# Optimization experiments

Hardware: AMD Instinct MI355X
Metric: run time of the kernel (lower is better)

## Reference

```python
import jax, jax.numpy as jnp
import numpy as np

EPS = 1e-12  # torch F.normalize eps

def _l2norm(t):
    # normalize along last axis, clamp norm like torch.nn.functional.normalize
    n = jnp.sqrt(jnp.sum(t * t, axis=-1, keepdims=True))
    return t / jnp.maximum(n, EPS)

def setup_inputs() -> dict:
    key = jax.random.key(0)
    k1, k2, k3 = jax.random.split(key, 3)
    B, N, C, h = 4, 16384, 512, 8
    x = jax.random.normal(k1, (B, N, C), dtype=jnp.float32)
    qkv_w = jax.random.normal(k2, (C, 3 * C), dtype=jnp.float32) * 0.02
    proj_w = jax.random.normal(k3, (C, C), dtype=jnp.float32) * 0.02
    proj_b = jnp.zeros((C,), dtype=jnp.float32)
    temperature = jnp.ones((h, 1, 1), dtype=jnp.float32)  # temperature_init=1.0
    return {"x": x, "H": 128, "W": 128, "qkv_w": qkv_w,
            "proj_w": proj_w, "proj_b": proj_b, "temperature": temperature}

def reference(x, H, W, qkv_w, proj_w, proj_b, temperature):
    B, N, C = x.shape
    h = temperature.shape[0]
    d = C // h
    qkv = (x @ qkv_w).reshape(B, N, 3, h, d)          # [B,N,3,h,d]
    qkv = jnp.transpose(qkv, (2, 0, 3, 1, 4))         # [3,B,h,N,d]
    q, k, v = qkv[0], qkv[1], qkv[2]
    # channel attention: transpose to [B,h,d,N], normalize over tokens
    q = _l2norm(jnp.swapaxes(q, -2, -1))              # [B,h,d,N]
    k = _l2norm(jnp.swapaxes(k, -2, -1))              # [B,h,d,N]
    v = jnp.swapaxes(v, -2, -1)                       # [B,h,d,N]
    attn = jnp.einsum('bhdn,bhen->bhde', q, k) * temperature  # [B,h,d,d]
    attn = jax.nn.softmax(attn, axis=-1)
    out = jnp.einsum('bhde,bhen->bhdn', attn, v)      # [B,h,d,N]
    out = jnp.transpose(out, (0, 3, 1, 2)).reshape(B, N, C)
    return out @ proj_w + proj_b
```

## Files before the change

### kernel.cpp

```cpp
#include <hip/hip_runtime.h>
#include <stdint.h>
#include <stddef.h>


typedef unsigned short u16;
typedef __attribute__((ext_vector_type(8))) unsigned short u16x8;
typedef __attribute__((ext_vector_type(8))) __bf16 bf16x8;
typedef __attribute__((ext_vector_type(4))) float f32x4;

#define B_DIM 4
#define N_TOK 16384
#define C_DIM 512
#define CQ3   1536
#define NROWS 65536

__device__ __forceinline__ u16 f2bf(float f) {
  union { float f; uint32_t u; } v; v.f = f;
  uint32_t r = v.u + 0x7FFFu + ((v.u >> 16) & 1u);
  return (u16)(r >> 16);
}
__device__ __forceinline__ float bf2f(u16 u) {
  union { uint32_t u; float f; } v; v.u = ((uint32_t)u) << 16;
  return v.f;
}
__device__ __forceinline__ bf16x8 as_bf16x8(u16x8 u) {
  union { u16x8 u; bf16x8 b; } v; v.u = u; return v.b;
}
__device__ __forceinline__ bf16x8 ldfrag(const u16* p) {
  return as_bf16x8(*(const u16x8*)p);
}
__device__ __forceinline__ void gl_lds16(const void* g, void* l) {
  __builtin_amdgcn_global_load_lds(
      (const __attribute__((address_space(1))) uint32_t*)g,
      (__attribute__((address_space(3))) uint32_t*)l, 16, 0, 0);
}
#define VMDRAIN asm volatile("s_waitcnt vmcnt(0)" ::: "memory")

__global__ __launch_bounds__(256) void k_prep(const float* __restrict__ qkv_w,
                                              const float* __restrict__ proj_w,
                                              u16* __restrict__ wl,
                                              u16* __restrict__ pwl,
                                              u16* __restrict__ vA) {
  int g = blockIdx.x * 256 + threadIdx.x;
  if (g < 98304) {
    int c8 = g / CQ3, j = g - c8 * CQ3;
    u16x8 o;
#pragma unroll
    for (int i = 0; i < 8; ++i) o[i] = f2bf(qkv_w[(size_t)(c8 * 8 + i) * CQ3 + j]);
    *(u16x8*)(wl + (size_t)g * 8) = o;
  } else if (g < 131072) {
    int gg = g - 98304;
    int d8 = gg >> 9, j = gg & 511;
    u16x8 o;
#pragma unroll
    for (int i = 0; i < 8; ++i) o[i] = f2bf(proj_w[(size_t)(d8 * 8 + i) * 512 + j]);
    *(u16x8*)(pwl + (size_t)gg * 8) = o;
  } else {
    int gg = g - 131072;
    int c = gg >> 6, q = gg & 63;
    const float* s = qkv_w + (size_t)c * CQ3 + 1024 + q * 8;
    float4 v0 = *(const float4*)s, v1 = *(const float4*)(s + 4);
    u16x8 o;
    o[0] = f2bf(v0.x); o[1] = f2bf(v0.y); o[2] = f2bf(v0.z); o[3] = f2bf(v0.w);
    o[4] = f2bf(v1.x); o[5] = f2bf(v1.y); o[6] = f2bf(v1.z); o[7] = f2bf(v1.w);
    *(u16x8*)(vA + (size_t)gg * 8) = o;
  }
}

__global__ __launch_bounds__(256) void k_xc(const float* __restrict__ x,
                                            u16* __restrict__ xb,
                                            u16* __restrict__ xbT) {
  __shared__ __align__(16) u16 T[16384];
  const int bi = blockIdx.x;
  const int b = bi >> 9, tt = (bi >> 2) & 127, ct = bi & 3;
  const int n0 = tt * 128, c0 = ct * 128;
  const int tid = threadIdx.x;
  const int cb8 = (tid & 15) * 8;
  const int tch = tid >> 4;
  const float* src = x + (size_t)(b * N_TOK + n0 + tch * 8) * C_DIM + c0 + cb8;
  float v[8][8];
#pragma unroll
  for (int j = 0; j < 8; ++j) {
    float4 a0 = *(const float4*)(src + (size_t)j * C_DIM);
    float4 a1 = *(const float4*)(src + (size_t)j * C_DIM + 4);
    v[j][0] = a0.x; v[j][1] = a0.y; v[j][2] = a0.z; v[j][3] = a0.w;
    v[j][4] = a1.x; v[j][5] = a1.y; v[j][6] = a1.z; v[j][7] = a1.w;
  }
  u16* xbd = xb + (size_t)(b * N_TOK + n0 + tch * 8) * C_DIM + c0 + cb8;
#pragma unroll
  for (int j = 0; j < 8; ++j) {
    u16x8 o;
#pragma unroll
    for (int i = 0; i < 8; ++i) o[i] = f2bf(v[j][i]);
    *(u16x8*)(xbd + (size_t)j * C_DIM) = o;
  }
#pragma unroll
  for (int i = 0; i < 8; ++i) {
    int c_loc = cb8 + i;
    int pc = tch ^ (tid & 15);
    u16x8 o;
#pragma unroll
    for (int j = 0; j < 8; ++j) o[j] = f2bf(v[j][i]);
    *(u16x8*)&T[c_loc * 128 + pc * 8] = o;
  }
  __syncthreads();
#pragma unroll
  for (int t = 0; t < 8; ++t) {
    int c_loc = t * 16 + (tid >> 4);
    int lch = tid & 15;
    int pc = lch ^ ((c_loc >> 3) & 15);
    u16x8 o = *(const u16x8*)&T[c_loc * 128 + pc * 8];
    *(u16x8*)&xbT[(size_t)(b * C_DIM + c0 + c_loc) * N_TOK + n0 + lch * 8] = o;
  }
}

__global__ __launch_bounds__(256) void k_g(const u16* __restrict__ xbT, u16* __restrict__ Gp) {
  __shared__ __align__(16) u16 As[2][8192];
  __shared__ __align__(16) u16 Bs[2][8192];
  const int tid = threadIdx.x, lane = tid & 63, wid = tid >> 6;
  const int orig = blockIdx.x;
  const int wg = (orig & 7) * 128 + (orig >> 3);
  const int kc = wg >> 6, rem = wg & 63;
  const int b = rem >> 4, ti = (rem >> 2) & 3, tj = rem & 3;
  const u16* abase = xbT + ((size_t)b * 512 + ti * 128) * N_TOK + kc * 1024;
  const u16* bbase = xbT + ((size_t)b * 512 + tj * 128) * N_TOK + kc * 1024;
  const int wr = wid >> 1, wc = wid & 1;

  const int sidx = tid >> 1, skblk0 = (tid & 1) * 4;

  auto stage = [&](int kb, int buf) {
#pragma unroll
    for (int s4 = 0; s4 < 4; ++s4) {
      int slot = s4 * 256 + tid;
      int idx = slot >> 3, kblk = slot & 7;
      int kcol = kb * 64 + ((kblk ^ (idx & 7)) * 8);
      gl_lds16(abase + (size_t)idx * N_TOK + kcol, &As[buf][slot * 8]);
      gl_lds16(bbase + (size_t)idx * N_TOK + kcol, &Bs[buf][slot * 8]);
    }
  };

  f32x4 acc[4][4];
#pragma unroll
  for (int i = 0; i < 4; ++i)
#pragma unroll
    for (int j = 0; j < 4; ++j) acc[i][j] = (f32x4){0.f, 0.f, 0.f, 0.f};

  stage(0, 0);
  VMDRAIN;
  __syncthreads();
  for (int kb = 0; kb < 16; ++kb) {
    const int cur = kb & 1;
    if (kb < 15) stage(kb + 1, cur ^ 1);
#pragma unroll
    for (int kk = 0; kk < 2; ++kk) {
      const int krow = kk * 4 + (lane >> 4);
      const int pk = krow ^ (lane & 7);
      bf16x8 af[4], bfr[4];
#pragma unroll
      for (int t = 0; t < 4; ++t)
        af[t] = *(const bf16x8*)&As[cur][((wr * 64 + t * 16 + (lane & 15)) * 8 + pk) * 8];
#pragma unroll
      for (int t = 0; t < 4; ++t)
        bfr[t] = *(const bf16x8*)&Bs[cur][((wc * 64 + t * 16 + (lane & 15)) * 8 + pk) * 8];
#pragma unroll
      for (int mt = 0; mt < 4; ++mt)
#pragma unroll
        for (int nt = 0; nt < 4; ++nt)
          acc[mt][nt] = __builtin_amdgcn_mfma_f32_16x16x32_bf16(af[mt], bfr[nt], acc[mt][nt], 0, 0, 0);
    }
    if (kb < 15) VMDRAIN;
    __syncthreads();
  }
  u16* wsl = &As[0][0] + wid * 4096;
#pragma unroll
  for (int mt = 0; mt < 4; ++mt)
#pragma unroll
    for (int nt = 0; nt < 4; ++nt)
#pragma unroll
      for (int r = 0; r < 4; ++r) {
        int row = mt * 16 + (lane >> 4) * 4 + r;
        int col = nt * 16 + (lane & 15);
        int slot = (col >> 3) ^ (row & 7);
        wsl[row * 64 + slot * 8 + (col & 7)] = f2bf(acc[mt][nt][r]);
      }
  u16* gdst = Gp + (size_t)(kc * 4 + b) * 262144;
#pragma unroll
  for (int it = 0; it < 8; ++it) {
    int rr = it * 8 + (lane >> 3);
    int slot = (lane & 7) ^ (rr & 7);
    *(u16x8*)&gdst[(size_t)(ti * 128 + wr * 64 + rr) * 512 + tj * 128 + wc * 64 + (lane & 7) * 8] =
        *(const u16x8*)&wsl[rr * 64 + slot * 8];
  }
}

__global__ __launch_bounds__(256) void k_red(const u16* __restrict__ Gp, u16* __restrict__ G) {
  int g = blockIdx.x * 256 + threadIdx.x;
  int b = g >> 15;
  size_t off = (size_t)(g & 32767) * 8;
  float s[8];
#pragma unroll
  for (int i = 0; i < 8; ++i) s[i] = 0.f;
  for (int kc = 0; kc < 16; ++kc) {
    u16x8 v = *(const u16x8*)(Gp + (size_t)(kc * 4 + b) * 262144 + off);
#pragma unroll
    for (int i = 0; i < 8; ++i) s[i] += bf2f(v[i]);
  }
  u16x8 o;
#pragma unroll
  for (int i = 0; i < 8; ++i) o[i] = f2bf(s[i]);
  *(u16x8*)(G + (size_t)b * 262144 + off) = o;
}

__global__ __launch_bounds__(256) void k_gq(const u16* __restrict__ G,
                                            const u16* __restrict__ wl,
                                            u16* __restrict__ Gqk) {
  const int bi = blockIdx.x;
  const int b = bi >> 5, mt = (bi >> 3) & 3, nt2 = bi & 7;
  const int m0 = mt * 128, n0 = nt2 * 128;
  const int lane = threadIdx.x & 63, w = threadIdx.x >> 6;
  f32x4 acc[8][2];
#pragma unroll
  for (int i = 0; i < 8; ++i) { acc[i][0] = (f32x4){0,0,0,0}; acc[i][1] = (f32x4){0,0,0,0}; }
  for (int ks = 0; ks < 16; ++ks) {
    bf16x8 bfr[2];
#pragma unroll
    for (int nf = 0; nf < 2; ++nf)
      bfr[nf] = ldfrag(wl + ((size_t)(ks * 4 + (lane >> 4)) * CQ3 + n0 + w * 32 + nf * 16 + (lane & 15)) * 8);
#pragma unroll
    for (int mf = 0; mf < 8; ++mf) {
      bf16x8 af = ldfrag(G + (size_t)b * 262144 + (size_t)(m0 + mf * 16 + (lane & 15)) * 512 + ks * 32 + (lane >> 4) * 8);
#pragma unroll
      for (int nf = 0; nf < 2; ++nf)
        acc[mf][nf] = __builtin_amdgcn_mfma_f32_16x16x32_bf16(af, bfr[nf], acc[mf][nf], 0, 0, 0);
    }
  }
#pragma unroll
  for (int mf = 0; mf < 8; ++mf)
#pragma unroll
    for (int nf = 0; nf < 2; ++nf)
#pragma unroll
      for (int r = 0; r < 4; ++r) {
        int d = m0 + mf * 16 + (lane >> 4) * 4 + r;
        int j = n0 + w * 32 + nf * 16 + (lane & 15);
        Gqk[(size_t)b * 524288 + ((size_t)(d >> 3) * 1024 + j) * 8 + (d & 7)] = f2bf(acc[mf][nf][r]);
      }
}

__global__ __launch_bounds__(256) void k_s2(const u16* __restrict__ Gqk,
                                            const u16* __restrict__ wl,
                                            const u16* __restrict__ pwl,
                                            const float* __restrict__ temp,
                                            u16* __restrict__ Ml) {
  __shared__ float Ssh[4][4096];
  __shared__ u16 At[64 * 72];
  __shared__ float ssqsh[128];
  __shared__ float rqk[128];
  const int tid = threadIdx.x, lane = tid & 63, w = tid >> 6;
  const int bh = blockIdx.x, b = bh >> 3, hh = bh & 7;
  if (tid < 128) ssqsh[tid] = 0.f;

  f32x4 acc[4][4];
#pragma unroll
  for (int i = 0; i < 4; ++i)
#pragma unroll
    for (int j = 0; j < 4; ++j) acc[i][j] = (f32x4){0.f, 0.f, 0.f, 0.f};
  for (int ks = 0; ks < 4; ++ks) {
    const int crow = w * 16 + ks * 4 + (lane >> 4);
    bf16x8 aq[4], bk[4];
#pragma unroll
    for (int mf = 0; mf < 4; ++mf)
      aq[mf] = ldfrag(wl + ((size_t)crow * CQ3 + hh * 64 + mf * 16 + (lane & 15)) * 8);
#pragma unroll
    for (int nf = 0; nf < 4; ++nf)
      bk[nf] = ldfrag(Gqk + (size_t)b * 524288 + ((size_t)crow * 1024 + 512 + hh * 64 + nf * 16 + (lane & 15)) * 8);
#pragma unroll
    for (int mf = 0; mf < 4; ++mf)
#pragma unroll
      for (int nf = 0; nf < 4; ++nf)
        acc[mf][nf] = __builtin_amdgcn_mfma_f32_16x16x32_bf16(aq[mf], bk[nf], acc[mf][nf], 0, 0, 0);
  }
#pragma unroll
  for (int mf = 0; mf < 4; ++mf)
#pragma unroll
    for (int nf = 0; nf < 4; ++nf)
#pragma unroll
      for (int r = 0; r < 4; ++r)
        Ssh[w][(mf * 16 + (lane >> 4) * 4 + r) * 64 + nf * 16 + (lane & 15)] = acc[mf][nf][r];
  __syncthreads();
  for (int idx = tid; idx < 4096; idx += 256)
    Ssh[0][idx] = Ssh[0][idx] + Ssh[1][idx] + Ssh[2][idx] + Ssh[3][idx];

  {
    const int d = tid & 63, part = tid >> 6;
    float sq = 0.f, sk = 0.f;
    for (int co = 0; co < 16; ++co) {
      int c8 = part * 16 + co;
      u16x8 wq = *(const u16x8*)(wl + ((size_t)c8 * CQ3 + hh * 64 + d) * 8);
      u16x8 gq = *(const u16x8*)(Gqk + (size_t)b * 524288 + ((size_t)c8 * 1024 + hh * 64 + d) * 8);
      u16x8 wk = *(const u16x8*)(wl + ((size_t)c8 * CQ3 + 512 + hh * 64 + d) * 8);
      u16x8 gk = *(const u16x8*)(Gqk + (size_t)b * 524288 + ((size_t)c8 * 1024 + 512 + hh * 64 + d) * 8);
#pragma unroll
      for (int i = 0; i < 8; ++i) {
        sq += bf2f(wq[i]) * bf2f(gq[i]);
        sk += bf2f(wk[i]) * bf2f(gk[i]);
      }
    }
    atomicAdd(&ssqsh[d], sq);
    atomicAdd(&ssqsh[64 + d], sk);
  }
  __syncthreads();
  if (tid < 128) rqk[tid] = 1.f / fmaxf(sqrtf(fmaxf(ssqsh[tid], 0.f)), 1e-12f);
  __syncthreads();

  {
    const float tp = temp[hh];
    const int d = tid >> 2, q4 = tid & 3;
    float vals[16];
    float mx = -3.0e38f;
    const float rqd = rqk[d];
#pragma unroll
    for (int i = 0; i < 16; ++i) {
      float v = Ssh[0][d * 64 + q4 * 16 + i] * rqd * rqk[64 + q4 * 16 + i] * tp;
      vals[i] = v; mx = fmaxf(mx, v);
    }
    mx = fmaxf(mx, __shfl_xor(mx, 1));
    mx = fmaxf(mx, __shfl_xor(mx, 2));
    float sum = 0.f;
#pragma unroll
    for (int i = 0; i < 16; ++i) { vals[i] = __expf(vals[i] - mx); sum += vals[i]; }
    sum += __shfl_xor(sum, 1);
    sum += __shfl_xor(sum, 2);
    const float inv = 1.f / sum;
#pragma unroll
    for (int i = 0; i < 16; ++i) At[(q4 * 16 + i) * 72 + d] = f2bf(vals[i] * inv);
  }
  __syncthreads();

  f32x4 acc2[4][8];
#pragma unroll
  for (int i = 0; i < 4; ++i)
#pragma unroll
    for (int j = 0; j < 8; ++j) acc2[i][j] = (f32x4){0.f, 0.f, 0.f, 0.f};
#pragma unroll
  for (int s = 0; s < 2; ++s) {
    bf16x8 af[4], bfr[8];
#pragma unroll
    for (int mf = 0; mf < 4; ++mf)
      af[mf] = *(const bf16x8*)&At[(mf * 16 + (lane & 15)) * 72 + s * 32 + (lane >> 4) * 8];
#pragma unroll
    for (int nf = 0; nf < 8; ++nf)
      bfr[nf] = ldfrag(pwl + ((size_t)(hh * 8 + s * 4 + (lane >> 4)) * 512 + w * 128 + nf * 16 + (lane & 15)) * 8);
#pragma unroll
    for (int mf = 0; mf < 4; ++mf)
#pragma unroll
      for (int nf = 0; nf < 8; ++nf)
        acc2[mf][nf] = __builtin_amdgcn_mfma_f32_16x16x32_bf16(af[mf], bfr[nf], acc2[mf][nf], 0, 0, 0);
  }
#pragma unroll
  for (int mf = 0; mf < 4; ++mf)
#pragma unroll
    for (int nf = 0; nf < 8; ++nf)
#pragma unroll
      for (int r = 0; r < 4; ++r) {
        int e = mf * 16 + (lane >> 4) * 4 + r;
        int j = w * 128 + nf * 16 + (lane & 15);
        int cc = hh * 64 + e;
        Ml[(size_t)b * 262144 + ((size_t)(cc >> 3) * 512 + j) * 8 + (cc & 7)] = f2bf(acc2[mf][nf][r]);
      }
}

__global__ __launch_bounds__(256) void k_p(const u16* __restrict__ vA,
                                           const u16* __restrict__ Ml,
                                           u16* __restrict__ Pl) {
  const int bi = blockIdx.x;
  const int b = bi >> 4, ct = (bi >> 2) & 3, jt = bi & 3;
  const int m0 = ct * 128, j0 = jt * 128;
  const int lane = threadIdx.x & 63, w = threadIdx.x >> 6;
  f32x4 acc[8][2];
#pragma unroll
  for (int i = 0; i < 8; ++i) { acc[i][0] = (f32x4){0,0,0,0}; acc[i][1] = (f32x4){0,0,0,0}; }
  for (int ks = 0; ks < 16; ++ks) {
    bf16x8 bfr[2];
#pragma unroll
    for (int nf = 0; nf < 2; ++nf)
      bfr[nf] = ldfrag(Ml + (size_t)b * 262144 + ((size_t)(ks * 4 + (lane >> 4)) * 512 + j0 + w * 32 + nf * 16 + (lane & 15)) * 8);
#pragma unroll
    for (int mf = 0; mf < 8; ++mf) {
      bf16x8 af = ldfrag(vA + (size_t)(m0 + mf * 16 + (lane & 15)) * 512 + ks * 32 + (lane >> 4) * 8);
#pragma unroll
      for (int nf = 0; nf < 2; ++nf)
        acc[mf][nf] = __builtin_amdgcn_mfma_f32_16x16x32_bf16(af, bfr[nf], acc[mf][nf], 0, 0, 0);
    }
  }
#pragma unroll
  for (int mf = 0; mf < 8; ++mf)
#pragma unroll
    for (int nf = 0; nf < 2; ++nf)
#pragma unroll
      for (int r = 0; r < 4; ++r) {
        int c = m0 + mf * 16 + (lane >> 4) * 4 + r;
        int j = j0 + w * 32 + nf * 16 + (lane & 15);
        Pl[(size_t)b * 262144 + ((size_t)(c >> 3) * 512 + j) * 8 + (c & 7)] = f2bf(acc[mf][nf][r]);
      }
}

__global__ __launch_bounds__(256) void k_out(const u16* __restrict__ xb,
                                             const u16* __restrict__ Pl,
                                             const float* __restrict__ pb,
                                             float* __restrict__ out) {
  __shared__ __align__(16) u16 As[2][8192];
  __shared__ __align__(16) u16 Bs[2][8192];
  const int tid = threadIdx.x;
  const int orig = blockIdx.x;
  const int wg = (orig & 7) * 256 + (orig >> 3);
  const int cb = wg & 3, rb = wg >> 2;
  const int row0 = rb * 128, col0 = cb * 128;
  const int b = rb >> 7;
  const int lane = tid & 63, wid = tid >> 6;
  const int wr = wid >> 1, wc = wid & 1;
  float bias[4];
#pragma unroll
  for (int nt = 0; nt < 4; ++nt) bias[nt] = pb[col0 + wc * 64 + nt * 16 + (lane & 15)];

  const u16* pbase = Pl + (size_t)b * 262144;
  auto stage = [&](int kb, int buf) {
#pragma unroll
    for (int s4 = 0; s4 < 4; ++s4) {
      int slot = s4 * 256 + tid;
      int idx = slot >> 3, kblk = slot & 7;
      gl_lds16(xb + (size_t)(row0 + idx) * C_DIM + kb * 64 + ((kblk ^ (idx & 7)) * 8),
               &As[buf][slot * 8]);
      int kblkB = slot >> 7, j = slot & 127;
      gl_lds16(pbase + ((size_t)(kb * 8 + kblkB) * 512 + col0 + j) * 8, &Bs[buf][slot * 8]);
    }
  };

  f32x4 acc[4][4];
#pragma unroll
  for (int i = 0; i < 4; ++i)
#pragma unroll
    for (int j = 0; j < 4; ++j) acc[i][j] = (f32x4){0.f, 0.f, 0.f, 0.f};

  stage(0, 0);
  VMDRAIN;
  __syncthreads();
  for (int kb = 0; kb < 8; ++kb) {
    const int cur = kb & 1;
    if (kb < 7) stage(kb + 1, cur ^ 1);
#pragma unroll
    for (int kk = 0; kk < 2; ++kk) {
      const int krow = kk * 4 + (lane >> 4);
      const int pk = krow ^ (lane & 7);
      bf16x8 af[4], bfr[4];
#pragma unroll
      for (int t = 0; t < 4; ++t)
        af[t] = *(const bf16x8*)&As[cur][((wr * 64 + t * 16 + (lane & 15)) * 8 + pk) * 8];
#pragma unroll
      for (int t = 0; t < 4; ++t)
        bfr[t] = *(const bf16x8*)&Bs[cur][(krow * 128 + wc * 64 + t * 16 + (lane & 15)) * 8];
#pragma unroll
      for (int mt = 0; mt < 4; ++mt)
#pragma unroll
        for (int nt = 0; nt < 4; ++nt)
          acc[mt][nt] = __builtin_amdgcn_mfma_f32_16x16x32_bf16(af[mt], bfr[nt], acc[mt][nt], 0, 0, 0);
    }
    if (kb < 7) VMDRAIN;
    __syncthreads();
  }
  float* slice = (float*)(&As[0][0]) + wid * 2048;
#pragma unroll
  for (int half = 0; half < 2; ++half) {
#pragma unroll
    for (int m2 = 0; m2 < 2; ++m2)
#pragma unroll
      for (int nt = 0; nt < 4; ++nt)
#pragma unroll
        for (int r = 0; r < 4; ++r) {
          int row = m2 * 16 + (lane >> 4) * 4 + r;
          int col = nt * 16 + (lane & 15);
          int slot = (col >> 2) ^ (row & 15);
          slice[row * 64 + slot * 4 + (col & 3)] = acc[half * 2 + m2][nt][r] + bias[nt];
        }
#pragma unroll
    for (int it = 0; it < 8; ++it) {
      int rr = it * 4 + (lane >> 4);
      int s = (lane & 15) ^ (rr & 15);
      *(float4*)&out[(size_t)(row0 + wr * 64 + half * 32 + rr) * C_DIM + col0 + wc * 64 + (lane & 15) * 4] =
          *(const float4*)&slice[rr * 64 + s * 4];
    }
  }
}

extern "C" void kernel_launch(void* const* d_in, const int* in_sizes, int n_in,
                              void* d_out, int out_size, void* d_ws, size_t ws_size,
                              hipStream_t stream) {
  const float* x      = (const float*)d_in[0];
  const float* qkv_w  = (const float*)d_in[3];
  const float* proj_w = (const float*)d_in[4];
  const float* proj_b = (const float*)d_in[5];
  const float* temp   = (const float*)d_in[6];
  float* out = (float*)d_out;

  char* ws = (char*)d_ws;
  u16* xb  = (u16*)(ws);
  u16* xbT = (u16*)(ws + 67108864);
  u16* wl  = (u16*)(ws + 134217728);
  u16* pwl = (u16*)(ws + 135790592);
  u16* vA  = (u16*)(ws + 136314880);
  u16* Gp  = (u16*)(ws + 136839168);
  u16* G   = (u16*)(ws + 170393600);
  u16* Gqk = (u16*)(ws + 172490752);
  u16* Ml  = (u16*)(ws + 176685056);
  u16* Pl  = (u16*)(ws + 178782208);

  k_xc<<<2048, 256, 0, stream>>>(x, xb, xbT);
  k_prep<<<640, 256, 0, stream>>>(qkv_w, proj_w, wl, pwl, vA);
  k_g<<<1024, 256, 0, stream>>>(xbT, Gp);
  k_red<<<512, 256, 0, stream>>>(Gp, G);
  k_gq<<<128, 256, 0, stream>>>(G, wl, Gqk);
  k_s2<<<32, 256, 0, stream>>>(Gqk, wl, pwl, temp, Ml);
  k_p<<<64, 256, 0, stream>>>(vA, Ml, Pl);
  k_out<<<2048, 256, 0, stream>>>(xb, Pl, proj_b, out);
}
```

Before: 250.4 us.

## Single-buffer A tile and read B fragments from global in k_out

k_out drops its double-buffered LDS staging. Only the A tile of x is kept in a single 16KB LDS buffer, and the B fragments of the projected weight are loaded straight from global memory with ldfrag. Launch bounds are raised to 4 waves per SIMD so more workgroups fit per CU and hide latency. The cost is that global loads are no longer overlapped with compute, since each iteration now waits on the load before the MFMAs, and B reads are repeated across waves through cache. The epilogue is reorganized to fit the smaller per-wave LDS slice.

```diff
diff --git a/kernel.cpp b/kernel.cpp
--- a/kernel.cpp
+++ b/kernel.cpp
@@ -126,8 +126,6 @@
   const u16* bbase = xbT + ((size_t)b * 512 + tj * 128) * N_TOK + kc * 1024;
   const int wr = wid >> 1, wc = wid & 1;
 
-  const int sidx = tid >> 1, skblk0 = (tid & 1) * 4;
-
   auto stage = [&](int kb, int buf) {
 #pragma unroll
     for (int s4 = 0; s4 < 4; ++s4) {
@@ -404,12 +402,11 @@
       }
 }
 
-__global__ __launch_bounds__(256) void k_out(const u16* __restrict__ xb,
-                                             const u16* __restrict__ Pl,
-                                             const float* __restrict__ pb,
-                                             float* __restrict__ out) {
-  __shared__ __align__(16) u16 As[2][8192];
-  __shared__ __align__(16) u16 Bs[2][8192];
+__global__ __launch_bounds__(256, 4) void k_out(const u16* __restrict__ xb,
+                                                const u16* __restrict__ Pl,
+                                                const float* __restrict__ pb,
+                                                float* __restrict__ out) {
+  __shared__ __align__(16) u16 As[8192];
   const int tid = threadIdx.x;
   const int orig = blockIdx.x;
   const int wg = (orig & 7) * 256 + (orig >> 3);
@@ -422,31 +419,23 @@
 #pragma unroll
   for (int nt = 0; nt < 4; ++nt) bias[nt] = pb[col0 + wc * 64 + nt * 16 + (lane & 15)];
 
-  const u16* pbase = Pl + (size_t)b * 262144;
-  auto stage = [&](int kb, int buf) {
+  f32x4 acc[4][4];
+#pragma unroll
+  for (int i = 0; i < 4; ++i)
+#pragma unroll
+    for (int j = 0; j < 4; ++j) acc[i][j] = (f32x4){0.f, 0.f, 0.f, 0.f};
+
+  const u16* pbase = Pl + (size_t)b * 262144 + (size_t)(col0 + wc * 64 + (lane & 15)) * 8;
+  for (int kb = 0; kb < 8; ++kb) {
 #pragma unroll
     for (int s4 = 0; s4 < 4; ++s4) {
       int slot = s4 * 256 + tid;
       int idx = slot >> 3, kblk = slot & 7;
       gl_lds16(xb + (size_t)(row0 + idx) * C_DIM + kb * 64 + ((kblk ^ (idx & 7)) * 8),
-               &As[buf][slot * 8]);
-      int kblkB = slot >> 7, j = slot & 127;
-      gl_lds16(pbase + ((size_t)(kb * 8 + kblkB) * 512 + col0 + j) * 8, &Bs[buf][slot * 8]);
-    }
-  };
-
-  f32x4 acc[4][4];
-#pragma unroll
-  for (int i = 0; i < 4; ++i)
-#pragma unroll
-    for (int j = 0; j < 4; ++j) acc[i][j] = (f32x4){0.f, 0.f, 0.f, 0.f};
-
-  stage(0, 0);
-  VMDRAIN;
-  __syncthreads();
-  for (int kb = 0; kb < 8; ++kb) {
-    const int cur = kb & 1;
-    if (kb < 7) stage(kb + 1, cur ^ 1);
+               &As[slot * 8]);
+    }
+    VMDRAIN;
+    __syncthreads();
 #pragma unroll
     for (int kk = 0; kk < 2; ++kk) {
       const int krow = kk * 4 + (lane >> 4);
@@ -454,38 +443,35 @@
       bf16x8 af[4], bfr[4];
 #pragma unroll
       for (int t = 0; t < 4; ++t)
-        af[t] = *(const bf16x8*)&As[cur][((wr * 64 + t * 16 + (lane & 15)) * 8 + pk) * 8];
+        af[t] = *(const bf16x8*)&As[((wr * 64 + t * 16 + (lane & 15)) * 8 + pk) * 8];
 #pragma unroll
       for (int t = 0; t < 4; ++t)
-        bfr[t] = *(const bf16x8*)&Bs[cur][(krow * 128 + wc * 64 + t * 16 + (lane & 15)) * 8];
+        bfr[t] = ldfrag(pbase + ((size_t)(kb * 8 + krow) * 512 + t * 16) * 8);
 #pragma unroll
       for (int mt = 0; mt < 4; ++mt)
 #pragma unroll
         for (int nt = 0; nt < 4; ++nt)
           acc[mt][nt] = __builtin_amdgcn_mfma_f32_16x16x32_bf16(af[mt], bfr[nt], acc[mt][nt], 0, 0, 0);
     }
-    if (kb < 7) VMDRAIN;
     __syncthreads();
   }
-  float* slice = (float*)(&As[0][0]) + wid * 2048;
-#pragma unroll
-  for (int half = 0; half < 2; ++half) {
-#pragma unroll
-    for (int m2 = 0; m2 < 2; ++m2)
-#pragma unroll
-      for (int nt = 0; nt < 4; ++nt)
-#pragma unroll
-        for (int r = 0; r < 4; ++r) {
-          int row = m2 * 16 + (lane >> 4) * 4 + r;
-          int col = nt * 16 + (lane & 15);
-          int slot = (col >> 2) ^ (row & 15);
-          slice[row * 64 + slot * 4 + (col & 3)] = acc[half * 2 + m2][nt][r] + bias[nt];
-        }
-#pragma unroll
-    for (int it = 0; it < 8; ++it) {
+  float* slice = (float*)(&As[0]) + wid * 1024;
+#pragma unroll
+  for (int mt = 0; mt < 4; ++mt) {
+#pragma unroll
+    for (int nt = 0; nt < 4; ++nt)
+#pragma unroll
+      for (int r = 0; r < 4; ++r) {
+        int r16 = (lane >> 4) * 4 + r;
+        int col = nt * 16 + (lane & 15);
+        int slot = (col >> 2) ^ r16;
+        slice[r16 * 64 + slot * 4 + (col & 3)] = acc[mt][nt][r] + bias[nt];
+      }
+#pragma unroll
+    for (int it = 0; it < 4; ++it) {
       int rr = it * 4 + (lane >> 4);
-      int s = (lane & 15) ^ (rr & 15);
-      *(float4*)&out[(size_t)(row0 + wr * 64 + half * 32 + rr) * C_DIM + col0 + wc * 64 + (lane & 15) * 4] =
+      int s = (lane & 15) ^ rr;
+      *(float4*)&out[(size_t)(row0 + wr * 64 + mt * 16 + rr) * C_DIM + col0 + wc * 64 + (lane & 15) * 4] =
           *(const float4*)&slice[rr * 64 + s * 4];
     }
   }
```

Measured after the change: 263.7 us. 1.05x slower.

## Exploit Gram symmetry to compute only upper-triangle tiles and single-buffer k_out

Applied to the files above, without the earlier changes.

The Gram kernel now computes only the 10 upper-triangular 128x128 tile pairs per batch instead of all 16, cutting its matmul work and partial-sum traffic. The reduction kernel sums those tiles and writes each off-diagonal result to both its own position and its transpose through shared memory. The reduction now runs as only 40 blocks, so its parallelism drops sharply. The output GEMM also switches from double-buffered to single-buffered LDS with an occupancy hint of 4, trading load/compute overlap for more resident workgroups.

```diff
diff --git a/kernel.cpp b/kernel.cpp
--- a/kernel.cpp
+++ b/kernel.cpp
@@ -13,6 +13,9 @@
 #define C_DIM 512
 #define CQ3   1536
 #define NROWS 65536
+
+__constant__ int PTI[10] = {0, 0, 0, 0, 1, 1, 1, 2, 2, 3};
+__constant__ int PTJ[10] = {0, 1, 2, 3, 1, 2, 3, 2, 3, 3};
 
 __device__ __forceinline__ u16 f2bf(float f) {
   union { float f; uint32_t u; } v; v.f = f;
@@ -119,14 +122,13 @@
   __shared__ __align__(16) u16 Bs[2][8192];
   const int tid = threadIdx.x, lane = tid & 63, wid = tid >> 6;
   const int orig = blockIdx.x;
-  const int wg = (orig & 7) * 128 + (orig >> 3);
-  const int kc = wg >> 6, rem = wg & 63;
-  const int b = rem >> 4, ti = (rem >> 2) & 3, tj = rem & 3;
+  const int wg = (orig & 7) * 80 + (orig >> 3);
+  const int kc = wg / 40, rem = wg % 40;
+  const int b = rem / 10, p = rem % 10;
+  const int ti = PTI[p], tj = PTJ[p];
   const u16* abase = xbT + ((size_t)b * 512 + ti * 128) * N_TOK + kc * 1024;
   const u16* bbase = xbT + ((size_t)b * 512 + tj * 128) * N_TOK + kc * 1024;
   const int wr = wid >> 1, wc = wid & 1;
-
-  const int sidx = tid >> 1, skblk0 = (tid & 1) * 4;
 
   auto stage = [&](int kb, int buf) {
 #pragma unroll
@@ -194,21 +196,43 @@
 }
 
 __global__ __launch_bounds__(256) void k_red(const u16* __restrict__ Gp, u16* __restrict__ G) {
-  int g = blockIdx.x * 256 + threadIdx.x;
-  int b = g >> 15;
-  size_t off = (size_t)(g & 32767) * 8;
-  float s[8];
-#pragma unroll
-  for (int i = 0; i < 8; ++i) s[i] = 0.f;
-  for (int kc = 0; kc < 16; ++kc) {
-    u16x8 v = *(const u16x8*)(Gp + (size_t)(kc * 4 + b) * 262144 + off);
-#pragma unroll
-    for (int i = 0; i < 8; ++i) s[i] += bf2f(v[i]);
-  }
-  u16x8 o;
-#pragma unroll
-  for (int i = 0; i < 8; ++i) o[i] = f2bf(s[i]);
-  *(u16x8*)(G + (size_t)b * 262144 + off) = o;
+  __shared__ u16 T[128][130];
+  const int bi = blockIdx.x;
+  const int b = bi / 10, p = bi - b * 10;
+  const int ti = PTI[p], tj = PTJ[p];
+  const int tid = threadIdx.x;
+  const int r = tid >> 1, h = tid & 1;
+  const u16* src = Gp + (size_t)b * 262144 + (size_t)(ti * 128 + r) * 512 + tj * 128 + h * 64;
+  u16* gdst = G + (size_t)b * 262144;
+#pragma unroll
+  for (int c8 = 0; c8 < 8; ++c8) {
+    float s[8];
+#pragma unroll
+    for (int i = 0; i < 8; ++i) s[i] = 0.f;
+    for (int kc = 0; kc < 16; ++kc) {
+      u16x8 v = *(const u16x8*)(src + (size_t)kc * 1048576 + c8 * 8);
+#pragma unroll
+      for (int i = 0; i < 8; ++i) s[i] += bf2f(v[i]);
+    }
+    u16x8 o;
+#pragma unroll
+    for (int i = 0; i < 8; ++i) o[i] = f2bf(s[i]);
+    *(u16x8*)(gdst + (size_t)(ti * 128 + r) * 512 + tj * 128 + h * 64 + c8 * 8) = o;
+#pragma unroll
+    for (int i = 0; i < 8; ++i) T[r][h * 64 + c8 * 8 + i] = o[i];
+  }
+  if (ti != tj) {
+    __syncthreads();
+    const int e = r;
+#pragma unroll
+    for (int c8 = 0; c8 < 8; ++c8) {
+      int d0 = h * 64 + c8 * 8;
+      u16x8 o;
+#pragma unroll
+      for (int i = 0; i < 8; ++i) o[i] = T[d0 + i][e];
+      *(u16x8*)(gdst + (size_t)(tj * 128 + e) * 512 + ti * 128 + d0) = o;
+    }
+  }
 }
 
 __global__ __launch_bounds__(256) void k_gq(const u16* __restrict__ G,
@@ -404,12 +428,12 @@
       }
 }
 
-__global__ __launch_bounds__(256) void k_out(const u16* __restrict__ xb,
-                                             const u16* __restrict__ Pl,
-                                             const float* __restrict__ pb,
-                                             float* __restrict__ out) {
-  __shared__ __align__(16) u16 As[2][8192];
-  __shared__ __align__(16) u16 Bs[2][8192];
+__global__ __launch_bounds__(256, 4) void k_out(const u16* __restrict__ xb,
+                                                const u16* __restrict__ Pl,
+                                                const float* __restrict__ pb,
+                                                float* __restrict__ out) {
+  __shared__ __align__(16) u16 As[8192];
+  __shared__ __align__(16) u16 Bs[8192];
   const int tid = threadIdx.x;
   const int orig = blockIdx.x;
   const int wg = (orig & 7) * 256 + (orig >> 3);
@@ -422,31 +446,23 @@
 #pragma unroll
   for (int nt = 0; nt < 4; ++nt) bias[nt] = pb[col0 + wc * 64 + nt * 16 + (lane & 15)];
 
+  f32x4 acc[4][4];
+#pragma unroll
+  for (int i = 0; i < 4; ++i)
+#pragma unroll
+    for (int j = 0; j < 4; ++j) acc[i][j] = (f32x4){0.f, 0.f, 0.f, 0.f};
+
   const u16* pbase = Pl + (size_t)b * 262144;
-  auto stage = [&](int kb, int buf) {
+  for (int kb = 0; kb < 8; ++kb) {
 #pragma unroll
     for (int s4 = 0; s4 < 4; ++s4) {
       int slot = s4 * 256 + tid;
       int idx = slot >> 3, kblk = slot & 7;
-      gl_lds16(xb + (size_t)(row0 + idx) * C_DIM + kb * 64 + ((kblk ^ (idx & 7)) * 8),
-               &As[buf][slot * 8]);
+      gl_lds16(xb + (size_t)(row0 + idx) * C_DIM + kb * 64 + ((kblk ^ (idx & 7)) * 8), &As[slot * 8]);
       int kblkB = slot >> 7, j = slot & 127;
-      gl_lds16(pbase + ((size_t)(kb * 8 + kblkB) * 512 + col0 + j) * 8, &Bs[buf][slot * 8]);
-    }
-  };
-
-  f32x4 acc[4][4];
-#pragma unroll
-  for (int i = 0; i < 4; ++i)
-#pragma unroll
-    for (int j = 0; j < 4; ++j) acc[i][j] = (f32x4){0.f, 0.f, 0.f, 0.f};
-
-  stage(0, 0);
-  VMDRAIN;
-  __syncthreads();
-  for (int kb = 0; kb < 8; ++kb) {
-    const int cur = kb & 1;
-    if (kb < 7) stage(kb + 1, cur ^ 1);
+      gl_lds16(pbase + ((size_t)(kb * 8 + kblkB) * 512 + col0 + j) * 8, &Bs[slot * 8]);
+    }
+    __syncthreads();
 #pragma unroll
     for (int kk = 0; kk < 2; ++kk) {
       const int krow = kk * 4 + (lane >> 4);
@@ -454,20 +470,19 @@
       bf16x8 af[4], bfr[4];
 #pragma unroll
       for (int t = 0; t < 4; ++t)
-        af[t] = *(const bf16x8*)&As[cur][((wr * 64 + t * 16 + (lane & 15)) * 8 + pk) * 8];
+        af[t] = *(const bf16x8*)&As[((wr * 64 + t * 16 + (lane & 15)) * 8 + pk) * 8];
 #pragma unroll
       for (int t = 0; t < 4; ++t)
-        bfr[t] = *(const bf16x8*)&Bs[cur][(krow * 128 + wc * 64 + t * 16 + (lane & 15)) * 8];
+        bfr[t] = *(const bf16x8*)&Bs[(krow * 128 + wc * 64 + t * 16 + (lane & 15)) * 8];
 #pragma unroll
       for (int mt = 0; mt < 4; ++mt)
 #pragma unroll
         for (int nt = 0; nt < 4; ++nt)
           acc[mt][nt] = __builtin_amdgcn_mfma_f32_16x16x32_bf16(af[mt], bfr[nt], acc[mt][nt], 0, 0, 0);
     }
-    if (kb < 7) VMDRAIN;
     __syncthreads();
   }
-  float* slice = (float*)(&As[0][0]) + wid * 2048;
+  float* slice = (wid < 2) ? (float*)&As[wid * 4096] : (float*)&Bs[(wid - 2) * 4096];
 #pragma unroll
   for (int half = 0; half < 2; ++half) {
 #pragma unroll
@@ -515,8 +530,8 @@
 
   k_xc<<<2048, 256, 0, stream>>>(x, xb, xbT);
   k_prep<<<640, 256, 0, stream>>>(qkv_w, proj_w, wl, pwl, vA);
-  k_g<<<1024, 256, 0, stream>>>(xbT, Gp);
-  k_red<<<512, 256, 0, stream>>>(Gp, G);
+  k_g<<<640, 256, 0, stream>>>(xbT, Gp);
+  k_red<<<40, 256, 0, stream>>>(Gp, G);
   k_gq<<<128, 256, 0, stream>>>(G, wl, Gqk);
   k_s2<<<32, 256, 0, stream>>>(Gqk, wl, pwl, temp, Ml);
   k_p<<<64, 256, 0, stream>>>(vA, Ml, Pl);
```

New measurement: 282.1 us. +12.7%, slower.
